# Kernel tuning notes

Measured on AMD Instinct MI355X. Metric: run time of the kernel, lower is better.

The kernel has to match this reference:

```python
import jax, jax.numpy as jnp
import numpy as np

B, S, D = 4, 2048, 1024


def setup_inputs() -> dict:
    key = jax.random.key(0)
    k1, k2, k3, k4 = jax.random.split(key, 4)
    scale = 1.0 / np.sqrt(D)
    return {
        "X_emb": jax.random.normal(k1, (B, S, D), dtype=jnp.float32),
        "W_q": jax.random.normal(k2, (D, D), dtype=jnp.float32) * scale,
        "W_k": jax.random.normal(k3, (D, D), dtype=jnp.float32) * scale,
        "W_v": jax.random.normal(k4, (D, D), dtype=jnp.float32) * scale,
    }


def reference(X_emb, W_q, W_k, W_v):
    # nn.Linear(bias=False): x @ W.T
    Xq = jnp.einsum('bsd,ed->bse', X_emb, W_q)
    Xk = jnp.einsum('bsd,ed->bse', X_emb, W_k)
    Xv = jnp.einsum('bsd,ed->bse', X_emb, W_v)
    S_len = X_emb.shape[-2]
    # scores [B, S, S]; causal mask (strict upper triangle -> -inf)
    att = jnp.einsum('bqe,bke->bqk', Xq, Xk)
    causal = jnp.tril(jnp.ones((S_len, S_len), dtype=bool))
    att = jnp.where(causal, att, -jnp.inf)
    # note: original masks before scaling; -inf / sqrt(d) is still -inf
    att = att / jnp.sqrt(jnp.asarray(Xk.shape[-1], att.dtype))
    w = jax.nn.softmax(att, axis=-1)
    return jnp.einsum('bqk,bke->bqe', w, Xv)
```

## Files before the change

### kernel.cpp

```cpp
#include <hip/hip_runtime.h>
#include <stdint.h>
#include <math.h>

typedef __attribute__((ext_vector_type(8))) __bf16 bf16x8;
typedef __attribute__((ext_vector_type(4))) float f32x4;

__device__ __forceinline__ unsigned short f2bf(float f) {
    unsigned u = __float_as_uint(f);
    u += 0x7FFF + ((u >> 16) & 1);
    return (unsigned short)(u >> 16);
}

__global__ __launch_bounds__(256)
void f32_to_bf16_k(const float* __restrict__ in, unsigned short* __restrict__ out, int n4) {
    int i = blockIdx.x * blockDim.x + threadIdx.x;
    int stride = gridDim.x * blockDim.x;
    for (; i < n4; i += stride) {
        float4 v = reinterpret_cast<const float4*>(in)[i];
        ushort4 o;
        o.x = f2bf(v.x); o.y = f2bf(v.y); o.z = f2bf(v.z); o.w = f2bf(v.w);
        reinterpret_cast<ushort4*>(out)[i] = o;
    }
}

__global__ __launch_bounds__(256)
void w_convert_k(const float* __restrict__ Wq, const float* __restrict__ Wk,
                 const float* __restrict__ Wv, unsigned short* __restrict__ out, int n4) {
    const float* src = blockIdx.y == 0 ? Wq : (blockIdx.y == 1 ? Wk : Wv);
    unsigned short* dst = out + (size_t)blockIdx.y * n4 * 4;
    int i = blockIdx.x * blockDim.x + threadIdx.x;
    int stride = gridDim.x * blockDim.x;
    for (; i < n4; i += stride) {
        float4 v = reinterpret_cast<const float4*>(src)[i];
        ushort4 o;
        o.x = f2bf(v.x); o.y = f2bf(v.y); o.z = f2bf(v.z); o.w = f2bf(v.w);
        reinterpret_cast<ushort4*>(dst)[i] = o;
    }
}

__device__ __forceinline__ void gload16(const unsigned short* g, unsigned short* l) {
    __builtin_amdgcn_global_load_lds(
        (const __attribute__((address_space(1))) unsigned int*)g,
        (__attribute__((address_space(3))) unsigned int*)l, 16, 0, 0);
}

template <int BM, int BN, int WM, int WN, typename CT, bool TRIE, bool KLIM>
__global__ __launch_bounds__(256, 2)
void gemm8(const unsigned short* __restrict__ A, const unsigned short* __restrict__ B,
           CT* __restrict__ C, int lda, int ldb, int ldc, int K,
           long long sA, long long sB, long long sC, float scale)
{
    constexpr int FM  = BM / WM / 16;
    constexpr int FN  = BN / WN / 16;
    constexpr int ACH = BM * 8;
    constexpr int LPT = (BM + BN) * 8 / 256;

    const int nbx = gridDim.x;
    const int nwg = nbx * gridDim.y;
    const int orig = blockIdx.y * nbx + blockIdx.x;
    const int q8 = nwg >> 3, r8 = nwg & 7;
    const int xcd = orig & 7, idx = orig >> 3;
    const int work = (xcd < r8 ? xcd * (q8 + 1) : r8 * (q8 + 1) + (xcd - r8) * q8) + idx;

    int br, bc;
    if constexpr (TRIE) {
        int rr = (int)((sqrtf(8.0f * (float)work + 1.0f) - 1.0f) * 0.5f);
        while ((rr + 1) * (rr + 2) / 2 <= work) ++rr;
        while (rr * (rr + 1) / 2 > work) --rr;
        br = rr; bc = work - rr * (rr + 1) / 2;
    } else {
        br = work / nbx; bc = work % nbx;
    }

    A += (long long)blockIdx.z * sA;
    B += (long long)blockIdx.z * sB;
    C += (long long)blockIdx.z * sC;

    int kmax = K;
    if (KLIM) { int kl = (br + 1) * BM; kmax = kl < K ? kl : K; }

    __shared__ unsigned short As[2][BM * 64];
    __shared__ unsigned short Bs[2][BN * 64];

    const int t    = threadIdx.x;
    const int lane = t & 63;
    const int wid  = t >> 6;
    const int wm   = wid / WN;
    const int wn   = wid % WN;
    const int m0   = br * BM, n0 = bc * BN;
    const int rsel = lane & 15;
    const int gsel = lane >> 4;

    f32x4 acc[FM][FN];
#pragma unroll
    for (int m = 0; m < FM; ++m)
#pragma unroll
        for (int n = 0; n < FN; ++n) acc[m][n] = (f32x4){0.f, 0.f, 0.f, 0.f};

    auto stage = [&](int buf, int kt) {
        const int k0 = kt * 64;
#pragma unroll
        for (int i = 0; i < LPT; ++i) {
            int ci = i * 256 + t;
            if (ci < ACH) {
                int row = ci >> 3, cc = ci & 7;
                gload16(A + (long long)(m0 + row) * lda + k0 + ((cc ^ (row & 7)) * 8),
                        &As[buf][ci * 8]);
            } else {
                int cj = ci - ACH;
                int row = cj >> 3, cc = cj & 7;
                gload16(B + (long long)(n0 + row) * ldb + k0 + ((cc ^ (row & 7)) * 8),
                        &Bs[buf][cj * 8]);
            }
        }
    };

    const int nk = kmax >> 6;
    stage(0, 0);

    for (int kt = 0; kt < nk; ++kt) {
        const int c = kt & 1;
        __builtin_amdgcn_s_barrier();
        __builtin_amdgcn_sched_barrier(0);
        if (kt + 1 < nk) {
            stage(c ^ 1, kt + 1);
            asm volatile("s_waitcnt vmcnt(8)" ::: "memory");
        } else {
            asm volatile("s_waitcnt vmcnt(0)" ::: "memory");
        }
        __builtin_amdgcn_s_barrier();
        __builtin_amdgcn_sched_barrier(0);

        bf16x8 aF[FM][2], bF[FN][2];
#pragma unroll
        for (int m = 0; m < FM; ++m)
#pragma unroll
            for (int ks = 0; ks < 2; ++ks) {
                int r  = wm * (FM * 16) + m * 16 + rsel;
                int cc = ks * 4 + gsel;
                aF[m][ks] = *reinterpret_cast<const bf16x8*>(
                    &As[c][r * 64 + ((cc ^ (r & 7)) * 8)]);
            }
#pragma unroll
        for (int n = 0; n < FN; ++n)
#pragma unroll
            for (int ks = 0; ks < 2; ++ks) {
                int rb = wn * (FN * 16) + n * 16 + rsel;
                int cc = ks * 4 + gsel;
                bF[n][ks] = *reinterpret_cast<const bf16x8*>(
                    &Bs[c][rb * 64 + ((cc ^ (rb & 7)) * 8)]);
            }

        __builtin_amdgcn_s_setprio(1);
#pragma unroll
        for (int m = 0; m < FM; ++m)
#pragma unroll
            for (int n = 0; n < FN; ++n)
#pragma unroll
                for (int ks = 0; ks < 2; ++ks)
                    acc[m][n] = __builtin_amdgcn_mfma_f32_16x16x32_bf16(
                        aF[m][ks], bF[n][ks], acc[m][n], 0, 0, 0);
        __builtin_amdgcn_s_setprio(0);
    }

    const int rowl = (lane >> 4) * 4;
#pragma unroll
    for (int m = 0; m < FM; ++m) {
#pragma unroll
        for (int n = 0; n < FN; ++n) {
#pragma unroll
            for (int i = 0; i < 4; ++i) {
                int r  = m0 + wm * (FM * 16) + m * 16 + rowl + i;
                int cI = n0 + wn * (FN * 16) + n * 16 + rsel;
                float v = acc[m][n][i] * scale;
                if constexpr (sizeof(CT) == 2)
                    ((unsigned short*)C)[(long long)r * ldc + cI] = f2bf(v);
                else
                    ((float*)C)[(long long)r * ldc + cI] = v;
            }
        }
    }
}

__device__ __forceinline__ float waveMax(float v) {
#pragma unroll
    for (int o = 32; o > 0; o >>= 1) v = fmaxf(v, __shfl_xor(v, o, 64));
    return v;
}
__device__ __forceinline__ float waveSum(float v) {
#pragma unroll
    for (int o = 32; o > 0; o >>= 1) v += __shfl_xor(v, o, 64);
    return v;
}

__global__ __launch_bounds__(256)
void softmax_causal(const float* __restrict__ S, unsigned short* __restrict__ P, int Slen) {
    __shared__ float e[2048];
    __shared__ float red[4];
    long long row = blockIdx.x;
    int q = (int)(row % Slen);
    const float* srow = S + row * (long long)Slen;
    unsigned short* prow = P + row * (long long)Slen;
    int len = q + 1;
    int t = threadIdx.x;

    int nfull = len >> 2;
    float mx = -3.0e38f;
    for (int i = t; i < nfull; i += 256) {
        float4 v = reinterpret_cast<const float4*>(srow)[i];
        e[4 * i + 0] = v.x; e[4 * i + 1] = v.y;
        e[4 * i + 2] = v.z; e[4 * i + 3] = v.w;
        mx = fmaxf(fmaxf(fmaxf(mx, v.x), v.y), fmaxf(v.z, v.w));
    }
    if (t < (len & 3)) {
        float v = srow[nfull * 4 + t];
        e[nfull * 4 + t] = v;
        mx = fmaxf(mx, v);
    }
    mx = waveMax(mx);
    if ((t & 63) == 0) red[t >> 6] = mx;
    __syncthreads();
    mx = fmaxf(fmaxf(red[0], red[1]), fmaxf(red[2], red[3]));

    float sum = 0.f;
    for (int k = t; k < len; k += 256) {
        float v = __expf(e[k] - mx);
        e[k] = v;
        sum += v;
    }
    sum = waveSum(sum);
    __syncthreads();
    if ((t & 63) == 0) red[t >> 6] = sum;
    __syncthreads();
    sum = red[0] + red[1] + red[2] + red[3];
    float inv = 1.0f / sum;

    int wlim = ((q >> 7) + 1) << 7;
    __syncthreads();
    for (int i = t; i < (wlim >> 2); i += 256) {
        int k = 4 * i;
        ushort4 o;
        o.x = (k + 0 < len) ? f2bf(e[k + 0] * inv) : (unsigned short)0;
        o.y = (k + 1 < len) ? f2bf(e[k + 1] * inv) : (unsigned short)0;
        o.z = (k + 2 < len) ? f2bf(e[k + 2] * inv) : (unsigned short)0;
        o.w = (k + 3 < len) ? f2bf(e[k + 3] * inv) : (unsigned short)0;
        reinterpret_cast<ushort4*>(prow)[i] = o;
    }
}

extern "C" void kernel_launch(void* const* d_in, const int* in_sizes, int n_in,
                              void* d_out, int out_size, void* d_ws, size_t ws_size,
                              hipStream_t stream) {
    const int B = 4, S = 2048, D = 1024;
    const float* X  = (const float*)d_in[0];
    const float* Wq = (const float*)d_in[1];
    const float* Wk = (const float*)d_in[2];
    const float* Wv = (const float*)d_in[3];
    float* out = (float*)d_out;

    char* ws = (char*)d_ws;
    unsigned short* Xb  = (unsigned short*)ws; ws += (size_t)B * S * D * 2;
    unsigned short* Wqb = (unsigned short*)ws; ws += (size_t)D * D * 2;
    unsigned short* Wkb = (unsigned short*)ws; ws += (size_t)D * D * 2;
    unsigned short* Wvb = (unsigned short*)ws; ws += (size_t)D * D * 2;
    unsigned short* Qb  = (unsigned short*)ws; ws += (size_t)B * S * D * 2;
    unsigned short* Kb  = (unsigned short*)ws; ws += (size_t)B * S * D * 2;
    unsigned short* Vt  = (unsigned short*)ws; ws += (size_t)B * S * D * 2;
    float*          Sc  = (float*)ws;          ws += (size_t)B * S * S * 4;
    unsigned short* P   = (unsigned short*)ws; ws += (size_t)B * S * S * 2;

    f32_to_bf16_k<<<2048, 256, 0, stream>>>(X, Xb, B * S * D / 4);
    w_convert_k<<<dim3(512, 3), 256, 0, stream>>>(Wq, Wk, Wv, Wqb, D * D / 4);

    dim3 blk(256);
    gemm8<128, 128, 2, 2, unsigned short, false, false>
        <<<dim3(D / 128, B * S / 128, 2), blk, 0, stream>>>(
        Xb, Wqb, Qb, D, D, D, D, 0, (long long)D * D, (long long)B * S * D, 1.0f);

    gemm8<128, 128, 2, 2, unsigned short, false, false>
        <<<dim3(S / 128, D / 128, B), blk, 0, stream>>>(
        Wvb, Xb, Vt, D, D, S, D, 0, (long long)S * D, (long long)D * S, 1.0f);

    const int nbt = (S / 128) * (S / 128 + 1) / 2;
    gemm8<128, 128, 2, 2, float, true, false>
        <<<dim3(nbt, 1, B), blk, 0, stream>>>(
        Qb, Kb, Sc, D, D, S, D, (long long)S * D, (long long)S * D, (long long)S * S, 0.03125f);

    softmax_causal<<<B * S, 256, 0, stream>>>(Sc, P, S);

    gemm8<128, 128, 2, 2, float, false, true>
        <<<dim3(D / 128, S / 128, B), blk, 0, stream>>>(
        P, Vt, out, S, S, D, S, (long long)S * S, (long long)D * S, (long long)S * D, 1.0f);
}
```

Baseline: 175.0 us.

## Replace 128x128 GEMM with 256x256 tile, 8-wave kernel with interleaved half-tile pipeline

Replaces the generic 128x128 4-wave GEMM with a 256x256 tile kernel using 512 threads (8 waves, each computing 128x64). The K loop is split into quarter-tile MFMA phases that interleave LDS fragment reads, global-to-LDS prefetch of the next stage, and barriers, giving a finer-grained software pipeline. This aims to raise data reuse per loaded byte and hide load latency. Larger tiles reduce the block count (e.g. the projection GEMMs drop to a few hundred blocks and the causal score GEMM to 36 triangular tiles per batch), which risks underfilling the GPU and wasting more work on causal-diagonal tiles. The softmax write limit is rounded to 256 to match the new tile.

Result: slower. 202.6 us (+15.7%).

```diff
diff --git a/kernel.cpp b/kernel.cpp
--- a/kernel.cpp
+++ b/kernel.cpp
@@ -4,6 +4,8 @@
 
 typedef __attribute__((ext_vector_type(8))) __bf16 bf16x8;
 typedef __attribute__((ext_vector_type(4))) float f32x4;
+
+template <int V> struct ic { static constexpr int value = V; };
 
 __device__ __forceinline__ unsigned short f2bf(float f) {
     unsigned u = __float_as_uint(f);
@@ -44,17 +46,12 @@
         (__attribute__((address_space(3))) unsigned int*)l, 16, 0, 0);
 }
 
-template <int BM, int BN, int WM, int WN, typename CT, bool TRIE, bool KLIM>
-__global__ __launch_bounds__(256, 2)
-void gemm8(const unsigned short* __restrict__ A, const unsigned short* __restrict__ B,
-           CT* __restrict__ C, int lda, int ldb, int ldc, int K,
-           long long sA, long long sB, long long sC, float scale)
+template <typename CT, bool TRIE, bool KLIM>
+__global__ __launch_bounds__(512, 2)
+void gemm256(const unsigned short* __restrict__ A, const unsigned short* __restrict__ B,
+             CT* __restrict__ C, int lda, int ldb, int ldc, int K,
+             long long sA, long long sB, long long sC, float scale)
 {
-    constexpr int FM  = BM / WM / 16;
-    constexpr int FN  = BN / WN / 16;
-    constexpr int ACH = BM * 8;
-    constexpr int LPT = (BM + BN) * 8 / 256;
-
     const int nbx = gridDim.x;
     const int nwg = nbx * gridDim.y;
     const int orig = blockIdx.y * nbx + blockIdx.x;
@@ -77,108 +74,175 @@
     C += (long long)blockIdx.z * sC;
 
     int kmax = K;
-    if (KLIM) { int kl = (br + 1) * BM; kmax = kl < K ? kl : K; }
-
-    __shared__ unsigned short As[2][BM * 64];
-    __shared__ unsigned short Bs[2][BN * 64];
+    if (KLIM) { int kl = (br + 1) * 256; kmax = kl < K ? kl : K; }
+
+    __shared__ unsigned short As[2][256 * 64];
+    __shared__ unsigned short Bs[2][256 * 64];
 
     const int t    = threadIdx.x;
     const int lane = t & 63;
     const int wid  = t >> 6;
-    const int wm   = wid / WN;
-    const int wn   = wid % WN;
-    const int m0   = br * BM, n0 = bc * BN;
+    const int wm   = wid >> 2;
+    const int wn   = wid & 3;
+    const int m0   = br * 256, n0 = bc * 256;
     const int rsel = lane & 15;
     const int gsel = lane >> 4;
 
-    f32x4 acc[FM][FN];
-#pragma unroll
-    for (int m = 0; m < FM; ++m)
-#pragma unroll
-        for (int n = 0; n < FN; ++n) acc[m][n] = (f32x4){0.f, 0.f, 0.f, 0.f};
-
-    auto stage = [&](int buf, int kt) {
-        const int k0 = kt * 64;
-#pragma unroll
-        for (int i = 0; i < LPT; ++i) {
-            int ci = i * 256 + t;
-            if (ci < ACH) {
-                int row = ci >> 3, cc = ci & 7;
-                gload16(A + (long long)(m0 + row) * lda + k0 + ((cc ^ (row & 7)) * 8),
-                        &As[buf][ci * 8]);
-            } else {
-                int cj = ci - ACH;
-                int row = cj >> 3, cc = cj & 7;
-                gload16(B + (long long)(n0 + row) * ldb + k0 + ((cc ^ (row & 7)) * 8),
-                        &Bs[buf][cj * 8]);
+    f32x4 acc[8][4];
+#pragma unroll
+    for (int m = 0; m < 8; ++m)
+#pragma unroll
+        for (int n = 0; n < 4; ++n) acc[m][n] = (f32x4){0.f, 0.f, 0.f, 0.f};
+
+    auto stageA = [&](int buf, int h, int kt) {
+#pragma unroll
+        for (int i = 0; i < 2; ++i) {
+            int ci = i * 512 + t;
+            int row = ci >> 3, cc = ci & 7;
+            gload16(A + (long long)(m0 + h * 128 + row) * lda + kt * 64 + ((cc ^ (row & 7)) * 8),
+                    &As[buf][h * 8192 + ci * 8]);
+        }
+    };
+    auto stageB = [&](int buf, int h, int kt) {
+#pragma unroll
+        for (int i = 0; i < 2; ++i) {
+            int ci = i * 512 + t;
+            int row = ci >> 3, cc = ci & 7;
+            gload16(B + (long long)(n0 + h * 128 + row) * ldb + kt * 64 + ((cc ^ (row & 7)) * 8),
+                    &Bs[buf][h * 8192 + ci * 8]);
+        }
+    };
+
+    auto readA = [&](int buf, int mh, bf16x8 (&dst)[4][2]) {
+#pragma unroll
+        for (int mm = 0; mm < 4; ++mm)
+#pragma unroll
+            for (int ks = 0; ks < 2; ++ks) {
+                int r  = mh * 128 + wm * 64 + mm * 16 + rsel;
+                int cc = ks * 4 + gsel;
+                dst[mm][ks] = *reinterpret_cast<const bf16x8*>(
+                    &As[buf][r * 64 + ((cc ^ (r & 7)) * 8)]);
             }
-        }
-    };
-
-    const int nk = kmax >> 6;
-    stage(0, 0);
-
-    for (int kt = 0; kt < nk; ++kt) {
-        const int c = kt & 1;
-        __builtin_amdgcn_s_barrier();
-        __builtin_amdgcn_sched_barrier(0);
-        if (kt + 1 < nk) {
-            stage(c ^ 1, kt + 1);
-            asm volatile("s_waitcnt vmcnt(8)" ::: "memory");
+    };
+    auto readB = [&](int buf, int nh, bf16x8 (&dst)[2][2]) {
+#pragma unroll
+        for (int nn = 0; nn < 2; ++nn)
+#pragma unroll
+            for (int ks = 0; ks < 2; ++ks) {
+                int rb = nh * 128 + wn * 32 + nn * 16 + rsel;
+                int cc = ks * 4 + gsel;
+                dst[nn][ks] = *reinterpret_cast<const bf16x8*>(
+                    &Bs[buf][rb * 64 + ((cc ^ (rb & 7)) * 8)]);
+            }
+    };
+
+    auto mfma16 = [&](auto MH, auto NH, bf16x8 (&aF)[4][2], bf16x8 (&bF)[2][2]) {
+        constexpr int mh = decltype(MH)::value, nh = decltype(NH)::value;
+        __builtin_amdgcn_s_setprio(1);
+#pragma unroll
+        for (int mm = 0; mm < 4; ++mm)
+#pragma unroll
+            for (int nn = 0; nn < 2; ++nn)
+#pragma unroll
+                for (int ks = 0; ks < 2; ++ks)
+                    acc[mh * 4 + mm][nh * 2 + nn] = __builtin_amdgcn_mfma_f32_16x16x32_bf16(
+                        aF[mm][ks], bF[nn][ks], acc[mh * 4 + mm][nh * 2 + nn], 0, 0, 0);
+        __builtin_amdgcn_s_setprio(0);
+    };
+
+#define BARF()  do { __builtin_amdgcn_s_barrier(); __builtin_amdgcn_sched_barrier(0); } while (0)
+#define LGKM0() do { asm volatile("s_waitcnt lgkmcnt(0)" ::: "memory"); \
+                     __builtin_amdgcn_sched_barrier(0); } while (0)
+
+    const int nk  = kmax >> 6;
+    const int nkk = nk >> 1;
+
+    stageA(0, 0, 0); stageB(0, 0, 0); stageB(0, 1, 0); stageA(0, 1, 0);
+    stageA(1, 0, 1); stageB(1, 0, 1); stageB(1, 1, 1); stageA(1, 1, 1);
+    asm volatile("s_waitcnt vmcnt(0)" ::: "memory");
+    BARF();
+
+    bf16x8 aF[4][2], bF0[2][2], bF1[2][2];
+
+    for (int i = 0; i < nkk; ++i) {
+        const bool pf = (i + 1 < nkk);
+        const int t2 = 2 * i + 2, t3 = 2 * i + 3;
+        if (i) stageA(1, 1, 2 * i + 1);
+        readA(0, 0, aF); readB(0, 0, bF0);
+        __builtin_amdgcn_s_barrier();
+        LGKM0();
+        mfma16(ic<0>{}, ic<0>{}, aF, bF0);
+        BARF();
+        if (pf) stageA(0, 0, t2);
+        readB(0, 1, bF1);
+        __builtin_amdgcn_s_barrier();
+        LGKM0();
+        mfma16(ic<0>{}, ic<1>{}, aF, bF1);
+        BARF();
+        if (pf) stageB(0, 0, t2);
+        readA(0, 1, aF);
+        __builtin_amdgcn_s_barrier();
+        LGKM0();
+        mfma16(ic<1>{}, ic<1>{}, aF, bF1);
+        BARF();
+        if (pf) {
+            stageB(0, 1, t2);
+            asm volatile("s_waitcnt vmcnt(6)" ::: "memory");
         } else {
             asm volatile("s_waitcnt vmcnt(0)" ::: "memory");
         }
         __builtin_amdgcn_s_barrier();
         __builtin_amdgcn_sched_barrier(0);
-
-        bf16x8 aF[FM][2], bF[FN][2];
-#pragma unroll
-        for (int m = 0; m < FM; ++m)
-#pragma unroll
-            for (int ks = 0; ks < 2; ++ks) {
-                int r  = wm * (FM * 16) + m * 16 + rsel;
-                int cc = ks * 4 + gsel;
-                aF[m][ks] = *reinterpret_cast<const bf16x8*>(
-                    &As[c][r * 64 + ((cc ^ (r & 7)) * 8)]);
-            }
-#pragma unroll
-        for (int n = 0; n < FN; ++n)
-#pragma unroll
-            for (int ks = 0; ks < 2; ++ks) {
-                int rb = wn * (FN * 16) + n * 16 + rsel;
-                int cc = ks * 4 + gsel;
-                bF[n][ks] = *reinterpret_cast<const bf16x8*>(
-                    &Bs[c][rb * 64 + ((cc ^ (rb & 7)) * 8)]);
-            }
-
-        __builtin_amdgcn_s_setprio(1);
-#pragma unroll
-        for (int m = 0; m < FM; ++m)
-#pragma unroll
-            for (int n = 0; n < FN; ++n)
-#pragma unroll
-                for (int ks = 0; ks < 2; ++ks)
-                    acc[m][n] = __builtin_amdgcn_mfma_f32_16x16x32_bf16(
-                        aF[m][ks], bF[n][ks], acc[m][n], 0, 0, 0);
-        __builtin_amdgcn_s_setprio(0);
-    }
-
-    const int rowl = (lane >> 4) * 4;
-#pragma unroll
-    for (int m = 0; m < FM; ++m) {
-#pragma unroll
-        for (int n = 0; n < FN; ++n) {
-#pragma unroll
-            for (int i = 0; i < 4; ++i) {
-                int r  = m0 + wm * (FM * 16) + m * 16 + rowl + i;
-                int cI = n0 + wn * (FN * 16) + n * 16 + rsel;
-                float v = acc[m][n][i] * scale;
-                if constexpr (sizeof(CT) == 2)
-                    ((unsigned short*)C)[(long long)r * ldc + cI] = f2bf(v);
-                else
-                    ((float*)C)[(long long)r * ldc + cI] = v;
-            }
+        mfma16(ic<1>{}, ic<0>{}, aF, bF0);
+        BARF();
+        if (pf) stageA(0, 1, t2);
+        readA(1, 0, aF); readB(1, 0, bF0);
+        __builtin_amdgcn_s_barrier();
+        LGKM0();
+        mfma16(ic<0>{}, ic<0>{}, aF, bF0);
+        BARF();
+        if (pf) stageA(1, 0, t3);
+        readB(1, 1, bF1);
+        __builtin_amdgcn_s_barrier();
+        LGKM0();
+        mfma16(ic<0>{}, ic<1>{}, aF, bF1);
+        BARF();
+        if (pf) stageB(1, 0, t3);
+        readA(1, 1, aF);
+        __builtin_amdgcn_s_barrier();
+        LGKM0();
+        mfma16(ic<1>{}, ic<1>{}, aF, bF1);
+        BARF();
+        if (pf) {
+            stageB(1, 1, t3);
+            asm volatile("s_waitcnt vmcnt(6)" ::: "memory");
         }
+        __builtin_amdgcn_s_barrier();
+        __builtin_amdgcn_sched_barrier(0);
+        mfma16(ic<1>{}, ic<0>{}, aF, bF0);
+        BARF();
+    }
+#undef BARF
+#undef LGKM0
+
+    const int rowl = gsel * 4;
+#pragma unroll
+    for (int mh = 0; mh < 2; ++mh)
+#pragma unroll
+    for (int mm = 0; mm < 4; ++mm)
+#pragma unroll
+    for (int nh = 0; nh < 2; ++nh)
+#pragma unroll
+    for (int nn = 0; nn < 2; ++nn)
+#pragma unroll
+    for (int i2 = 0; i2 < 4; ++i2) {
+        int r  = m0 + mh * 128 + wm * 64 + mm * 16 + rowl + i2;
+        int cI = n0 + nh * 128 + wn * 32 + nn * 16 + rsel;
+        float v = acc[mh * 4 + mm][nh * 2 + nn][i2] * scale;
+        if constexpr (sizeof(CT) == 2)
+            ((unsigned short*)C)[(long long)r * ldc + cI] = f2bf(v);
+        else
+            ((float*)C)[(long long)r * ldc + cI] = v;
     }
 }
 
@@ -235,7 +299,7 @@
     sum = red[0] + red[1] + red[2] + red[3];
     float inv = 1.0f / sum;
 
-    int wlim = ((q >> 7) + 1) << 7;
+    int wlim = ((q >> 8) + 1) << 8;
     __syncthreads();
     for (int i = t; i < (wlim >> 2); i += 256) {
         int k = 4 * i;
@@ -272,23 +336,23 @@
     f32_to_bf16_k<<<2048, 256, 0, stream>>>(X, Xb, B * S * D / 4);
     w_convert_k<<<dim3(512, 3), 256, 0, stream>>>(Wq, Wk, Wv, Wqb, D * D / 4);
 
-    dim3 blk(256);
-    gemm8<128, 128, 2, 2, unsigned short, false, false>
-        <<<dim3(D / 128, B * S / 128, 2), blk, 0, stream>>>(
+    dim3 blk(512);
+    gemm256<unsigned short, false, false>
+        <<<dim3(D / 256, B * S / 256, 2), blk, 0, stream>>>(
         Xb, Wqb, Qb, D, D, D, D, 0, (long long)D * D, (long long)B * S * D, 1.0f);
 
-    gemm8<128, 128, 2, 2, unsigned short, false, false>
-        <<<dim3(S / 128, D / 128, B), blk, 0, stream>>>(
+    gemm256<unsigned short, false, false>
+        <<<dim3(S / 256, D / 256, B), blk, 0, stream>>>(
         Wvb, Xb, Vt, D, D, S, D, 0, (long long)S * D, (long long)D * S, 1.0f);
 
-    const int nbt = (S / 128) * (S / 128 + 1) / 2;
-    gemm8<128, 128, 2, 2, float, true, false>
+    const int nbt = (S / 256) * (S / 256 + 1) / 2;
+    gemm256<float, true, false>
         <<<dim3(nbt, 1, B), blk, 0, stream>>>(
         Qb, Kb, Sc, D, D, S, D, (long long)S * D, (long long)S * D, (long long)S * S, 0.03125f);
 
     softmax_causal<<<B * S, 256, 0, stream>>>(Sc, P, S);
 
-    gemm8<128, 128, 2, 2, float, false, true>
-        <<<dim3(D / 128, S / 128, B), blk, 0, stream>>>(
+    gemm256<float, false, true>
+        <<<dim3(D / 256, S / 256, B), blk, 0, stream>>>(
         P, Vt, out, S, S, D, S, (long long)S * S, (long long)D * S, (long long)S * D, 1.0f);
 }
```

## Balance causal GEMM workloads by pairing triangular tiles per workgroup

Applied to the files above, without the earlier changes.

The P·V GEMM now gives each workgroup two row-blocks (p and 15-p) with complementary causal K lengths, so every workgroup does equal work and the grid is halved. The QK^T triangular GEMM launches 128 workgroups per batch instead of 136, and a subset of workgroups picks up the 8 leftover tiles as a second tile. Both aim to remove load imbalance and tail effects from causal triangles. The cost is serialized tiles per workgroup, an extra barrier between tiles, and fewer, longer-running workgroups.

Result: slower. 178.9 us (+2.2%).

```diff
diff --git a/kernel.cpp b/kernel.cpp
--- a/kernel.cpp
+++ b/kernel.cpp
@@ -44,14 +44,14 @@
         (__attribute__((address_space(3))) unsigned int*)l, 16, 0, 0);
 }
 
-template <int BM, int BN, int WM, int WN, typename CT, bool TRIE, bool KLIM>
+template <typename CT, int MODE>
 __global__ __launch_bounds__(256, 2)
 void gemm8(const unsigned short* __restrict__ A, const unsigned short* __restrict__ B,
            CT* __restrict__ C, int lda, int ldb, int ldc, int K,
-           long long sA, long long sB, long long sC, float scale)
+           long long sA, long long sB, long long sC, float scale, int totj)
 {
-    constexpr int FM  = BM / WM / 16;
-    constexpr int FN  = BN / WN / 16;
+    constexpr int BM = 128, BN = 128;
+    constexpr int FM = 4, FN = 4;
     constexpr int ACH = BM * 8;
     constexpr int LPT = (BM + BN) * 8 / 256;
 
@@ -62,42 +62,21 @@
     const int xcd = orig & 7, idx = orig >> 3;
     const int work = (xcd < r8 ? xcd * (q8 + 1) : r8 * (q8 + 1) + (xcd - r8) * q8) + idx;
 
-    int br, bc;
-    if constexpr (TRIE) {
-        int rr = (int)((sqrtf(8.0f * (float)work + 1.0f) - 1.0f) * 0.5f);
-        while ((rr + 1) * (rr + 2) / 2 <= work) ++rr;
-        while (rr * (rr + 1) / 2 > work) --rr;
-        br = rr; bc = work - rr * (rr + 1) / 2;
-    } else {
-        br = work / nbx; bc = work % nbx;
-    }
-
     A += (long long)blockIdx.z * sA;
     B += (long long)blockIdx.z * sB;
     C += (long long)blockIdx.z * sC;
 
-    int kmax = K;
-    if (KLIM) { int kl = (br + 1) * BM; kmax = kl < K ? kl : K; }
-
     __shared__ unsigned short As[2][BM * 64];
     __shared__ unsigned short Bs[2][BN * 64];
 
     const int t    = threadIdx.x;
     const int lane = t & 63;
     const int wid  = t >> 6;
-    const int wm   = wid / WN;
-    const int wn   = wid % WN;
-    const int m0   = br * BM, n0 = bc * BN;
+    const int wm   = wid >> 1, wn = wid & 1;
     const int rsel = lane & 15;
     const int gsel = lane >> 4;
 
-    f32x4 acc[FM][FN];
-#pragma unroll
-    for (int m = 0; m < FM; ++m)
-#pragma unroll
-        for (int n = 0; n < FN; ++n) acc[m][n] = (f32x4){0.f, 0.f, 0.f, 0.f};
-
-    auto stage = [&](int buf, int kt) {
+    auto stage = [&](int buf, int kt, int m0, int n0) {
         const int k0 = kt * 64;
 #pragma unroll
         for (int i = 0; i < LPT; ++i) {
@@ -115,70 +94,107 @@
         }
     };
 
-    const int nk = kmax >> 6;
-    stage(0, 0);
-
-    for (int kt = 0; kt < nk; ++kt) {
-        const int c = kt & 1;
-        __builtin_amdgcn_s_barrier();
-        __builtin_amdgcn_sched_barrier(0);
-        if (kt + 1 < nk) {
-            stage(c ^ 1, kt + 1);
-            asm volatile("s_waitcnt vmcnt(8)" ::: "memory");
-        } else {
-            asm volatile("s_waitcnt vmcnt(0)" ::: "memory");
-        }
-        __builtin_amdgcn_s_barrier();
-        __builtin_amdgcn_sched_barrier(0);
-
-        bf16x8 aF[FM][2], bF[FN][2];
+    auto run_tile = [&](int br, int bc, int kmax, bool first) {
+        const int m0 = br * BM, n0 = bc * BN;
+        f32x4 acc[FM][FN];
 #pragma unroll
         for (int m = 0; m < FM; ++m)
 #pragma unroll
-            for (int ks = 0; ks < 2; ++ks) {
-                int r  = wm * (FM * 16) + m * 16 + rsel;
-                int cc = ks * 4 + gsel;
-                aF[m][ks] = *reinterpret_cast<const bf16x8*>(
-                    &As[c][r * 64 + ((cc ^ (r & 7)) * 8)]);
+            for (int n = 0; n < FN; ++n) acc[m][n] = (f32x4){0.f, 0.f, 0.f, 0.f};
+
+        const int nk = kmax >> 6;
+        if (!first) {
+            __builtin_amdgcn_s_barrier();
+            __builtin_amdgcn_sched_barrier(0);
+        }
+        stage(0, 0, m0, n0);
+
+        for (int kt = 0; kt < nk; ++kt) {
+            const int c = kt & 1;
+            __builtin_amdgcn_s_barrier();
+            __builtin_amdgcn_sched_barrier(0);
+            if (kt + 1 < nk) {
+                stage(c ^ 1, kt + 1, m0, n0);
+                asm volatile("s_waitcnt vmcnt(8)" ::: "memory");
+            } else {
+                asm volatile("s_waitcnt vmcnt(0)" ::: "memory");
             }
-#pragma unroll
-        for (int n = 0; n < FN; ++n)
-#pragma unroll
-            for (int ks = 0; ks < 2; ++ks) {
-                int rb = wn * (FN * 16) + n * 16 + rsel;
-                int cc = ks * 4 + gsel;
-                bF[n][ks] = *reinterpret_cast<const bf16x8*>(
-                    &Bs[c][rb * 64 + ((cc ^ (rb & 7)) * 8)]);
+            __builtin_amdgcn_s_barrier();
+            __builtin_amdgcn_sched_barrier(0);
+
+            bf16x8 aF[FM][2], bF[FN][2];
+#pragma unroll
+            for (int m = 0; m < FM; ++m)
+#pragma unroll
+                for (int ks = 0; ks < 2; ++ks) {
+                    int r  = wm * (FM * 16) + m * 16 + rsel;
+                    int cc = ks * 4 + gsel;
+                    aF[m][ks] = *reinterpret_cast<const bf16x8*>(
+                        &As[c][r * 64 + ((cc ^ (r & 7)) * 8)]);
+                }
+#pragma unroll
+            for (int n = 0; n < FN; ++n)
+#pragma unroll
+                for (int ks = 0; ks < 2; ++ks) {
+                    int rb = wn * (FN * 16) + n * 16 + rsel;
+                    int cc = ks * 4 + gsel;
+                    bF[n][ks] = *reinterpret_cast<const bf16x8*>(
+                        &Bs[c][rb * 64 + ((cc ^ (rb & 7)) * 8)]);
+                }
+
+            __builtin_amdgcn_s_setprio(1);
+#pragma unroll
+            for (int m = 0; m < FM; ++m)
+#pragma unroll
+                for (int n = 0; n < FN; ++n)
+#pragma unroll
+                    for (int ks = 0; ks < 2; ++ks)
+                        acc[m][n] = __builtin_amdgcn_mfma_f32_16x16x32_bf16(
+                            aF[m][ks], bF[n][ks], acc[m][n], 0, 0, 0);
+            __builtin_amdgcn_s_setprio(0);
+        }
+
+        const int rowl = gsel * 4;
+#pragma unroll
+        for (int m = 0; m < FM; ++m) {
+#pragma unroll
+            for (int n = 0; n < FN; ++n) {
+#pragma unroll
+                for (int i = 0; i < 4; ++i) {
+                    int r  = m0 + wm * (FM * 16) + m * 16 + rowl + i;
+                    int cI = n0 + wn * (FN * 16) + n * 16 + rsel;
+                    float v = acc[m][n][i] * scale;
+                    if constexpr (sizeof(CT) == 2)
+                        ((unsigned short*)C)[(long long)r * ldc + cI] = f2bf(v);
+                    else
+                        ((float*)C)[(long long)r * ldc + cI] = v;
+                }
             }
-
-        __builtin_amdgcn_s_setprio(1);
-#pragma unroll
-        for (int m = 0; m < FM; ++m)
-#pragma unroll
-            for (int n = 0; n < FN; ++n)
-#pragma unroll
-                for (int ks = 0; ks < 2; ++ks)
-                    acc[m][n] = __builtin_amdgcn_mfma_f32_16x16x32_bf16(
-                        aF[m][ks], bF[n][ks], acc[m][n], 0, 0, 0);
-        __builtin_amdgcn_s_setprio(0);
-    }
-
-    const int rowl = (lane >> 4) * 4;
-#pragma unroll
-    for (int m = 0; m < FM; ++m) {
-#pragma unroll
-        for (int n = 0; n < FN; ++n) {
-#pragma unroll
-            for (int i = 0; i < 4; ++i) {
-                int r  = m0 + wm * (FM * 16) + m * 16 + rowl + i;
-                int cI = n0 + wn * (FN * 16) + n * 16 + rsel;
-                float v = acc[m][n][i] * scale;
-                if constexpr (sizeof(CT) == 2)
-                    ((unsigned short*)C)[(long long)r * ldc + cI] = f2bf(v);
-                else
-                    ((float*)C)[(long long)r * ldc + cI] = v;
-            }
-        }
+        }
+    };
+
+    auto tri = [&](int w, int& br, int& bc) {
+        int rr = (int)((sqrtf(8.0f * (float)w + 1.0f) - 1.0f) * 0.5f);
+        while ((rr + 1) * (rr + 2) / 2 <= w) ++rr;
+        while (rr * (rr + 1) / 2 > w) --rr;
+        br = rr; bc = w - rr * (rr + 1) / 2;
+    };
+
+    if constexpr (MODE == 0) {
+        run_tile(work / nbx, work % nbx, K, true);
+    } else if constexpr (MODE == 1) {
+        int br, bc;
+        tri(work, br, bc);
+        run_tile(br, bc, K, true);
+        const int e = work >> 4;
+        if ((work & 15) == 8 && nwg + e < totj) {
+            tri(nwg + e, br, bc);
+            run_tile(br, bc, K, false);
+        }
+    } else {
+        const int p = work / nbx, bc = work % nbx;
+        run_tile(p, bc, (p + 1) * BM, true);
+        run_tile(totj - 1 - p, bc, (totj - p) * BM, false);
     }
 }
 
@@ -273,22 +289,19 @@
     w_convert_k<<<dim3(512, 3), 256, 0, stream>>>(Wq, Wk, Wv, Wqb, D * D / 4);
 
     dim3 blk(256);
-    gemm8<128, 128, 2, 2, unsigned short, false, false>
-        <<<dim3(D / 128, B * S / 128, 2), blk, 0, stream>>>(
-        Xb, Wqb, Qb, D, D, D, D, 0, (long long)D * D, (long long)B * S * D, 1.0f);
-
-    gemm8<128, 128, 2, 2, unsigned short, false, false>
-        <<<dim3(S / 128, D / 128, B), blk, 0, stream>>>(
-        Wvb, Xb, Vt, D, D, S, D, 0, (long long)S * D, (long long)D * S, 1.0f);
-
-    const int nbt = (S / 128) * (S / 128 + 1) / 2;
-    gemm8<128, 128, 2, 2, float, true, false>
-        <<<dim3(nbt, 1, B), blk, 0, stream>>>(
-        Qb, Kb, Sc, D, D, S, D, (long long)S * D, (long long)S * D, (long long)S * S, 0.03125f);
+    gemm8<unsigned short, 0><<<dim3(D / 128, B * S / 128, 2), blk, 0, stream>>>(
+        Xb, Wqb, Qb, D, D, D, D, 0, (long long)D * D, (long long)B * S * D, 1.0f, 0);
+
+    gemm8<unsigned short, 0><<<dim3(S / 128, D / 128, B), blk, 0, stream>>>(
+        Wvb, Xb, Vt, D, D, S, D, 0, (long long)S * D, (long long)D * S, 1.0f, 0);
+
+    gemm8<float, 1><<<dim3(8, 16, B), blk, 0, stream>>>(
+        Qb, Kb, Sc, D, D, S, D, (long long)S * D, (long long)S * D, (long long)S * S,
+        0.03125f, 136);
 
     softmax_causal<<<B * S, 256, 0, stream>>>(Sc, P, S);
 
-    gemm8<128, 128, 2, 2, float, false, true>
-        <<<dim3(D / 128, S / 128, B), blk, 0, stream>>>(
-        P, Vt, out, S, S, D, S, (long long)S * S, (long long)D * S, (long long)S * D, 1.0f);
-}
+    gemm8<float, 2><<<dim3(D / 128, 8, B), blk, 0, stream>>>(
+        P, Vt, out, S, S, D, S, (long long)S * S, (long long)D * S, (long long)S * D,
+        1.0f, 16);
+}
```
